# Optimization experiments

Hardware: AMD Instinct MI355X
Metric: run time of the kernel (lower is better)

The kernel has to match this reference:

```python
import jax, jax.numpy as jnp
import numpy as np

ALPHA = 32.0
RANK = 256
SCALE = ALPHA / RANK


def setup_inputs() -> dict:
    key = jax.random.key(0)
    k1, k2, k3, k4 = jax.random.split(key, 4)
    x = jax.random.normal(k1, (4, 2048, 4096), dtype=jnp.float32)
    A = jax.random.normal(k2, (256, 4096), dtype=jnp.float32)   # (rank, in)
    B = jax.random.normal(k3, (4096, 256), dtype=jnp.float32)   # (out, rank)
    d_A = jnp.ones((256,), dtype=jnp.float32)                    # init = ones (as in module)
    d_B = jax.random.normal(k4, (4096,), dtype=jnp.float32)      # perturbed for a nontrivial test
    return {"x": x, "A": A, "B": B, "d_A": d_A, "d_B": d_B}


def reference(x, A, B, d_A, d_B):
    # Effective weight: diag(d_B) @ B @ diag(d_A) @ A  -> (out, in)
    scaled_A = d_A[:, None] * A                 # (rank, in)
    BA = B @ scaled_A                            # (out, in)
    W_vera = d_B[:, None] * BA                   # (out, in)
    # out = x @ W_vera.T * scale  -> (..., out)
    return jnp.einsum('bsi,oi->bso', x, W_vera) * SCALE
```

## Files before the change

kernel.cpp:

```cpp
#include <hip/hip_runtime.h>
#include <hip/hip_bf16.h>


#define SCALE_F 0.125f
#define M_TOT 8192
#define K_IN 4096
#define RANK 256
#define N_OUT 4096
#define S_SPLIT 4
#define KC 1024

typedef __bf16 bf16_t;
typedef __bf16 bf16x8 __attribute__((ext_vector_type(8)));
typedef __bf16 bf16x4 __attribute__((ext_vector_type(4)));
typedef float f32x4 __attribute__((ext_vector_type(4)));

typedef __attribute__((address_space(3))) unsigned int lds_u32_t;
typedef const __attribute__((address_space(1))) unsigned int glob_u32_t;

__device__ __forceinline__ void async16(const void* g, void* l) {
    __builtin_amdgcn_global_load_lds((glob_u32_t*)g, (lds_u32_t*)l, 16, 0, 0);
}

__global__ __launch_bounds__(256) void conv_AB(const float* __restrict__ A,
                                               const float* __restrict__ dA,
                                               const float* __restrict__ B,
                                               bf16_t* __restrict__ Ab,
                                               bf16_t* __restrict__ Bb) {
    int b = blockIdx.x;
    if (b < 1024) {
        int idx = b * 256 + threadIdx.x;
        float4 v = ((const float4*)A)[idx];
        float s = dA[idx >> 10];
        bf16x4 o;
        o.x = (bf16_t)(v.x * s); o.y = (bf16_t)(v.y * s);
        o.z = (bf16_t)(v.z * s); o.w = (bf16_t)(v.w * s);
        ((bf16x4*)Ab)[idx] = o;
    } else {
        int idx = (b - 1024) * 256 + threadIdx.x;
        float4 v = ((const float4*)B)[idx];
        bf16x4 o;
        o.x = (bf16_t)v.x; o.y = (bf16_t)v.y;
        o.z = (bf16_t)v.z; o.w = (bf16_t)v.w;
        ((bf16x4*)Bb)[idx] = o;
    }
}

__global__ __launch_bounds__(256) void gemm1(const float* __restrict__ x,
                                             const bf16_t* __restrict__ Ab,
                                             bf16_t* __restrict__ part) {
    __shared__ bf16_t sX[2][64 * 64];
    __shared__ bf16_t sA[2][128 * 64];
    const int tid = threadIdx.x;
    const int lane = tid & 63, wave = tid >> 6;
    const int wm = wave >> 1, wn = wave & 1;
    const int l15 = lane & 15, quad = lane >> 4;
    const int bm = blockIdx.x * 64;
    const int bn = blockIdx.y * 128;
    const int k0 = blockIdx.z * KC;

    f32x4 acc[2][4];
    const f32x4 zero = {0.f, 0.f, 0.f, 0.f};
    #pragma unroll
    for (int i = 0; i < 2; i++)
        #pragma unroll
        for (int j = 0; j < 4; j++) acc[i][j] = zero;

    f32x4 xr[2][2];

    auto issue_x = [&](int kk) {
        #pragma unroll
        for (int c = 0; c < 2; c++) {
            int idx = c * 256 + tid;
            int row = idx >> 3, sl = idx & 7;
            const float* sp = &x[(size_t)(bm + row) * K_IN + kk + sl * 8];
            xr[c][0] = *(const f32x4*)sp;
            xr[c][1] = *(const f32x4*)(sp + 4);
        }
    };
    auto stage_a = [&](int b, int kk) {
        #pragma unroll
        for (int c = 0; c < 4; c++) {
            int idx = c * 256 + tid;
            int row = idx >> 3, sl = idx & 7;
            async16(&Ab[(size_t)(bn + row) * K_IN + kk + ((sl ^ (row & 7)) << 3)],
                    &sA[b][idx * 8]);
        }
    };
    auto write_x = [&](int b) {
        #pragma unroll
        for (int c = 0; c < 2; c++) {
            int idx = c * 256 + tid;
            int row = idx >> 3, sl = idx & 7;
            bf16x8 o;
            #pragma unroll
            for (int e = 0; e < 4; e++) {
                o[e]     = (bf16_t)xr[c][0][e];
                o[e + 4] = (bf16_t)xr[c][1][e];
            }
            *(bf16x8*)&sX[b][row * 64 + ((sl ^ (row & 7)) << 3)] = o;
        }
    };
    auto compute = [&](int b) {
        #pragma unroll
        for (int ks = 0; ks < 2; ks++) {
            bf16x8 af[2], bfr[4];
            #pragma unroll
            for (int i = 0; i < 2; i++) {
                int row = wm * 32 + i * 16 + l15;
                af[i] = *(const bf16x8*)&sX[b][row * 64 + ((((ks << 2) | quad) ^ (row & 7)) << 3)];
            }
            #pragma unroll
            for (int j = 0; j < 4; j++) {
                int row = wn * 64 + j * 16 + l15;
                bfr[j] = *(const bf16x8*)&sA[b][row * 64 + ((((ks << 2) | quad) ^ (row & 7)) << 3)];
            }
            #pragma unroll
            for (int i = 0; i < 2; i++)
                #pragma unroll
                for (int j = 0; j < 4; j++)
                    acc[i][j] = __builtin_amdgcn_mfma_f32_16x16x32_bf16(bfr[j], af[i], acc[i][j], 0, 0, 0);
        }
    };

    issue_x(k0);
    stage_a(0, k0);
    write_x(0);
    __syncthreads();

    int cur = 0;
    for (int it = 1; it < KC / 64; ++it) {
        const int nxt = cur ^ 1;
        const int kk = k0 + it * 64;
        issue_x(kk);
        stage_a(nxt, kk);
        compute(cur);
        write_x(nxt);
        __syncthreads();
        cur = nxt;
    }
    compute(cur);

    bf16_t* p = part + (size_t)blockIdx.z * (M_TOT * RANK);
    #pragma unroll
    for (int i = 0; i < 2; i++) {
        int row = bm + wm * 32 + i * 16 + l15;
        #pragma unroll
        for (int j = 0; j < 4; j++) {
            int col = bn + wn * 64 + j * 16 + quad * 4;
            bf16x4 o;
            #pragma unroll
            for (int r = 0; r < 4; r++) o[r] = (bf16_t)acc[i][j][r];
            *(bf16x4*)&p[(size_t)row * RANK + col] = o;
        }
    }
}

__global__ __launch_bounds__(256) void reduce_t(const bf16_t* __restrict__ part,
                                                bf16_t* __restrict__ t) {
    int i = (blockIdx.x * 256 + threadIdx.x) * 8;
    float s[8] = {0.f, 0.f, 0.f, 0.f, 0.f, 0.f, 0.f, 0.f};
    #pragma unroll
    for (int z = 0; z < S_SPLIT; z++) {
        bf16x8 v = *(const bf16x8*)&part[(size_t)z * M_TOT * RANK + i];
        #pragma unroll
        for (int e = 0; e < 8; e++) s[e] += (float)v[e];
    }
    bf16x8 o;
    #pragma unroll
    for (int e = 0; e < 8; e++) o[e] = (bf16_t)s[e];
    *(bf16x8*)&t[i] = o;
}

__global__ __launch_bounds__(256) void gemm2(const bf16_t* __restrict__ t,
                                             const bf16_t* __restrict__ Bb,
                                             const float* __restrict__ dB,
                                             float* __restrict__ out) {
    __shared__ bf16_t sT[2][128 * 64];
    __shared__ bf16_t sB[2][64 * 64];
    const int tid = threadIdx.x;
    const int lane = tid & 63, wave = tid >> 6;
    const int wm = wave >> 1, wn = wave & 1;
    const int l15 = lane & 15, quad = lane >> 4;
    const int bm = blockIdx.x * 128;
    const int bn = blockIdx.y * 64;

    f32x4 acc[4][2];
    const f32x4 zero = {0.f, 0.f, 0.f, 0.f};
    #pragma unroll
    for (int i = 0; i < 4; i++)
        #pragma unroll
        for (int j = 0; j < 2; j++) acc[i][j] = zero;

    auto stage = [&](int b, int kt) {
        #pragma unroll
        for (int c = 0; c < 4; c++) {
            int idx = c * 256 + tid;
            int row = idx >> 3, sl = idx & 7;
            async16(&t[(size_t)(bm + row) * RANK + kt + ((sl ^ (row & 7)) << 3)],
                    &sT[b][idx * 8]);
        }
        #pragma unroll
        for (int c = 0; c < 2; c++) {
            int idx = c * 256 + tid;
            int row = idx >> 3, sl = idx & 7;
            async16(&Bb[(size_t)(bn + row) * RANK + kt + ((sl ^ (row & 7)) << 3)],
                    &sB[b][idx * 8]);
        }
    };
    auto compute = [&](int b) {
        #pragma unroll
        for (int ks = 0; ks < 2; ks++) {
            bf16x8 af[4], bfr[2];
            #pragma unroll
            for (int i = 0; i < 4; i++) {
                int row = wm * 64 + i * 16 + l15;
                af[i] = *(const bf16x8*)&sT[b][row * 64 + ((((ks << 2) | quad) ^ (row & 7)) << 3)];
            }
            #pragma unroll
            for (int j = 0; j < 2; j++) {
                int row = wn * 32 + j * 16 + l15;
                bfr[j] = *(const bf16x8*)&sB[b][row * 64 + ((((ks << 2) | quad) ^ (row & 7)) << 3)];
            }
            #pragma unroll
            for (int i = 0; i < 4; i++)
                #pragma unroll
                for (int j = 0; j < 2; j++)
                    acc[i][j] = __builtin_amdgcn_mfma_f32_16x16x32_bf16(bfr[j], af[i], acc[i][j], 0, 0, 0);
        }
    };

    stage(0, 0);
    __syncthreads();
    int cur = 0;
    #pragma unroll
    for (int it = 1; it < RANK / 64; ++it) {
        stage(cur ^ 1, it * 64);
        compute(cur);
        __syncthreads();
        cur ^= 1;
    }
    compute(cur);

    #pragma unroll
    for (int i = 0; i < 4; i++) {
        int row = bm + wm * 64 + i * 16 + l15;
        #pragma unroll
        for (int j = 0; j < 2; j++) {
            int col = bn + wn * 32 + j * 16 + quad * 4;
            f32x4 db = *(const f32x4*)&dB[col];
            f32x4 o;
            #pragma unroll
            for (int r = 0; r < 4; r++) o[r] = db[r] * SCALE_F * acc[i][j][r];
            *(f32x4*)&out[(size_t)row * N_OUT + col] = o;
        }
    }
}

extern "C" void kernel_launch(void* const* d_in, const int* in_sizes, int n_in,
                              void* d_out, int out_size, void* d_ws, size_t ws_size,
                              hipStream_t stream) {
    const float* x  = (const float*)d_in[0];
    const float* A  = (const float*)d_in[1];
    const float* B  = (const float*)d_in[2];
    const float* dA = (const float*)d_in[3];
    const float* dB = (const float*)d_in[4];
    float* out = (float*)d_out;

    char* ws = (char*)d_ws;
    bf16_t* Ab   = (bf16_t*)ws;
    bf16_t* Bb   = (bf16_t*)(ws + (1u << 21));
    bf16_t* tt   = (bf16_t*)(ws + (1u << 22));
    bf16_t* part = (bf16_t*)(ws + (1u << 23));

    conv_AB<<<2048, 256, 0, stream>>>(A, dA, B, Ab, Bb);
    gemm1<<<dim3(128, 2, S_SPLIT), 256, 0, stream>>>(x, Ab, part);
    reduce_t<<<1024, 256, 0, stream>>>(part, tt);
    gemm2<<<dim3(64, 64), 256, 0, stream>>>(tt, Bb, dB, out);
}
```

Before: 319.7 us.

## Widen gemm1 tile to full rank and load whole K panel in gemm2

```diff
diff --git a/kernel.cpp b/kernel.cpp
--- a/kernel.cpp
+++ b/kernel.cpp
@@ -50,21 +50,20 @@
                                              const bf16_t* __restrict__ Ab,
                                              bf16_t* __restrict__ part) {
     __shared__ bf16_t sX[2][64 * 64];
-    __shared__ bf16_t sA[2][128 * 64];
+    __shared__ bf16_t sA[2][256 * 64];
     const int tid = threadIdx.x;
     const int lane = tid & 63, wave = tid >> 6;
     const int wm = wave >> 1, wn = wave & 1;
     const int l15 = lane & 15, quad = lane >> 4;
     const int bm = blockIdx.x * 64;
-    const int bn = blockIdx.y * 128;
-    const int k0 = blockIdx.z * KC;
-
-    f32x4 acc[2][4];
+    const int k0 = blockIdx.y * KC;
+
+    f32x4 acc[2][8];
     const f32x4 zero = {0.f, 0.f, 0.f, 0.f};
     #pragma unroll
     for (int i = 0; i < 2; i++)
         #pragma unroll
-        for (int j = 0; j < 4; j++) acc[i][j] = zero;
+        for (int j = 0; j < 8; j++) acc[i][j] = zero;
 
     f32x4 xr[2][2];
 
@@ -80,10 +79,10 @@
     };
     auto stage_a = [&](int b, int kk) {
         #pragma unroll
-        for (int c = 0; c < 4; c++) {
+        for (int c = 0; c < 8; c++) {
             int idx = c * 256 + tid;
             int row = idx >> 3, sl = idx & 7;
-            async16(&Ab[(size_t)(bn + row) * K_IN + kk + ((sl ^ (row & 7)) << 3)],
+            async16(&Ab[(size_t)row * K_IN + kk + ((sl ^ (row & 7)) << 3)],
                     &sA[b][idx * 8]);
         }
     };
@@ -104,21 +103,21 @@
     auto compute = [&](int b) {
         #pragma unroll
         for (int ks = 0; ks < 2; ks++) {
-            bf16x8 af[2], bfr[4];
+            bf16x8 af[2], bfr[8];
             #pragma unroll
             for (int i = 0; i < 2; i++) {
                 int row = wm * 32 + i * 16 + l15;
                 af[i] = *(const bf16x8*)&sX[b][row * 64 + ((((ks << 2) | quad) ^ (row & 7)) << 3)];
             }
             #pragma unroll
-            for (int j = 0; j < 4; j++) {
-                int row = wn * 64 + j * 16 + l15;
+            for (int j = 0; j < 8; j++) {
+                int row = wn * 128 + j * 16 + l15;
                 bfr[j] = *(const bf16x8*)&sA[b][row * 64 + ((((ks << 2) | quad) ^ (row & 7)) << 3)];
             }
             #pragma unroll
             for (int i = 0; i < 2; i++)
                 #pragma unroll
-                for (int j = 0; j < 4; j++)
+                for (int j = 0; j < 8; j++)
                     acc[i][j] = __builtin_amdgcn_mfma_f32_16x16x32_bf16(bfr[j], af[i], acc[i][j], 0, 0, 0);
         }
     };
@@ -141,13 +140,13 @@
     }
     compute(cur);
 
-    bf16_t* p = part + (size_t)blockIdx.z * (M_TOT * RANK);
+    bf16_t* p = part + (size_t)blockIdx.y * (M_TOT * RANK);
     #pragma unroll
     for (int i = 0; i < 2; i++) {
         int row = bm + wm * 32 + i * 16 + l15;
         #pragma unroll
-        for (int j = 0; j < 4; j++) {
-            int col = bn + wn * 64 + j * 16 + quad * 4;
+        for (int j = 0; j < 8; j++) {
+            int col = wn * 128 + j * 16 + quad * 4;
             bf16x4 o;
             #pragma unroll
             for (int r = 0; r < 4; r++) o[r] = (bf16_t)acc[i][j][r];
@@ -176,75 +175,57 @@
                                              const bf16_t* __restrict__ Bb,
                                              const float* __restrict__ dB,
                                              float* __restrict__ out) {
-    __shared__ bf16_t sT[2][128 * 64];
-    __shared__ bf16_t sB[2][64 * 64];
+    __shared__ bf16_t sT[64 * 256];
+    __shared__ bf16_t sB[64 * 256];
     const int tid = threadIdx.x;
     const int lane = tid & 63, wave = tid >> 6;
     const int wm = wave >> 1, wn = wave & 1;
     const int l15 = lane & 15, quad = lane >> 4;
-    const int bm = blockIdx.x * 128;
+    const int bm = blockIdx.x * 64;
     const int bn = blockIdx.y * 64;
 
-    f32x4 acc[4][2];
+    #pragma unroll
+    for (int c = 0; c < 8; c++) {
+        int idx = c * 256 + tid;
+        int row = idx >> 5, sl = idx & 31;
+        int src = ((sl ^ (row & 7)) << 3);
+        async16(&t[(size_t)(bm + row) * RANK + src], &sT[idx * 8]);
+        async16(&Bb[(size_t)(bn + row) * RANK + src], &sB[idx * 8]);
+    }
+    __syncthreads();
+
+    f32x4 acc[2][2];
     const f32x4 zero = {0.f, 0.f, 0.f, 0.f};
     #pragma unroll
-    for (int i = 0; i < 4; i++)
+    for (int i = 0; i < 2; i++)
         #pragma unroll
         for (int j = 0; j < 2; j++) acc[i][j] = zero;
 
-    auto stage = [&](int b, int kt) {
-        #pragma unroll
-        for (int c = 0; c < 4; c++) {
-            int idx = c * 256 + tid;
-            int row = idx >> 3, sl = idx & 7;
-            async16(&t[(size_t)(bm + row) * RANK + kt + ((sl ^ (row & 7)) << 3)],
-                    &sT[b][idx * 8]);
-        }
-        #pragma unroll
-        for (int c = 0; c < 2; c++) {
-            int idx = c * 256 + tid;
-            int row = idx >> 3, sl = idx & 7;
-            async16(&Bb[(size_t)(bn + row) * RANK + kt + ((sl ^ (row & 7)) << 3)],
-                    &sB[b][idx * 8]);
-        }
-    };
-    auto compute = [&](int b) {
-        #pragma unroll
-        for (int ks = 0; ks < 2; ks++) {
-            bf16x8 af[4], bfr[2];
-            #pragma unroll
-            for (int i = 0; i < 4; i++) {
-                int row = wm * 64 + i * 16 + l15;
-                af[i] = *(const bf16x8*)&sT[b][row * 64 + ((((ks << 2) | quad) ^ (row & 7)) << 3)];
-            }
-            #pragma unroll
-            for (int j = 0; j < 2; j++) {
-                int row = wn * 32 + j * 16 + l15;
-                bfr[j] = *(const bf16x8*)&sB[b][row * 64 + ((((ks << 2) | quad) ^ (row & 7)) << 3)];
-            }
-            #pragma unroll
-            for (int i = 0; i < 4; i++)
-                #pragma unroll
-                for (int j = 0; j < 2; j++)
-                    acc[i][j] = __builtin_amdgcn_mfma_f32_16x16x32_bf16(bfr[j], af[i], acc[i][j], 0, 0, 0);
-        }
-    };
-
-    stage(0, 0);
-    __syncthreads();
-    int cur = 0;
-    #pragma unroll
-    for (int it = 1; it < RANK / 64; ++it) {
-        stage(cur ^ 1, it * 64);
-        compute(cur);
-        __syncthreads();
-        cur ^= 1;
-    }
-    compute(cur);
-
-    #pragma unroll
-    for (int i = 0; i < 4; i++) {
-        int row = bm + wm * 64 + i * 16 + l15;
+    #pragma unroll
+    for (int ks = 0; ks < 8; ks++) {
+        bf16x8 af[2], bfr[2];
+        #pragma unroll
+        for (int i = 0; i < 2; i++) {
+            int row = wm * 32 + i * 16 + l15;
+            int slot = ((ks << 2) | quad) ^ (row & 7);
+            af[i] = *(const bf16x8*)&sT[row * 256 + slot * 8];
+        }
+        #pragma unroll
+        for (int j = 0; j < 2; j++) {
+            int row = wn * 32 + j * 16 + l15;
+            int slot = ((ks << 2) | quad) ^ (row & 7);
+            bfr[j] = *(const bf16x8*)&sB[row * 256 + slot * 8];
+        }
+        #pragma unroll
+        for (int i = 0; i < 2; i++)
+            #pragma unroll
+            for (int j = 0; j < 2; j++)
+                acc[i][j] = __builtin_amdgcn_mfma_f32_16x16x32_bf16(bfr[j], af[i], acc[i][j], 0, 0, 0);
+    }
+
+    #pragma unroll
+    for (int i = 0; i < 2; i++) {
+        int row = bm + wm * 32 + i * 16 + l15;
         #pragma unroll
         for (int j = 0; j < 2; j++) {
             int col = bn + wn * 32 + j * 16 + quad * 4;
@@ -274,7 +255,7 @@
     bf16_t* part = (bf16_t*)(ws + (1u << 23));
 
     conv_AB<<<2048, 256, 0, stream>>>(A, dA, B, Ab, Bb);
-    gemm1<<<dim3(128, 2, S_SPLIT), 256, 0, stream>>>(x, Ab, part);
+    gemm1<<<dim3(128, S_SPLIT), 256, 0, stream>>>(x, Ab, part);
     reduce_t<<<1024, 256, 0, stream>>>(part, tt);
-    gemm2<<<dim3(64, 64), 256, 0, stream>>>(tt, Bb, dB, out);
-}
+    gemm2<<<dim3(128, 64), 256, 0, stream>>>(tt, Bb, dB, out);
+}
```

Measured after the change: 338.5 us. +5.9%, slower.

## Stage fp32 x via async LDS loads with K=32 tiles and two-deep prefetch

Applied to the files above, without the earlier changes.

```diff
diff --git a/kernel.cpp b/kernel.cpp
--- a/kernel.cpp
+++ b/kernel.cpp
@@ -46,11 +46,11 @@
     }
 }
 
-__global__ __launch_bounds__(256) void gemm1(const float* __restrict__ x,
-                                             const bf16_t* __restrict__ Ab,
-                                             bf16_t* __restrict__ part) {
-    __shared__ bf16_t sX[2][64 * 64];
-    __shared__ bf16_t sA[2][128 * 64];
+__global__ __launch_bounds__(256, 4) void gemm1(const float* __restrict__ x,
+                                                const bf16_t* __restrict__ Ab,
+                                                bf16_t* __restrict__ part) {
+    __shared__ float  sXf[2][64 * 32];
+    __shared__ bf16_t sA[2][128 * 32];
     const int tid = threadIdx.x;
     const int lane = tid & 63, wave = tid >> 6;
     const int wm = wave >> 1, wn = wave & 1;
@@ -66,79 +66,65 @@
         #pragma unroll
         for (int j = 0; j < 4; j++) acc[i][j] = zero;
 
-    f32x4 xr[2][2];
-
-    auto issue_x = [&](int kk) {
+    auto stage = [&](int b, int ts) {
+        const int kk = k0 + ts * 32;
         #pragma unroll
         for (int c = 0; c < 2; c++) {
             int idx = c * 256 + tid;
             int row = idx >> 3, sl = idx & 7;
-            const float* sp = &x[(size_t)(bm + row) * K_IN + kk + sl * 8];
-            xr[c][0] = *(const f32x4*)sp;
-            xr[c][1] = *(const f32x4*)(sp + 4);
-        }
-    };
-    auto stage_a = [&](int b, int kk) {
-        #pragma unroll
-        for (int c = 0; c < 4; c++) {
-            int idx = c * 256 + tid;
-            int row = idx >> 3, sl = idx & 7;
-            async16(&Ab[(size_t)(bn + row) * K_IN + kk + ((sl ^ (row & 7)) << 3)],
-                    &sA[b][idx * 8]);
-        }
-    };
-    auto write_x = [&](int b) {
+            async16(&x[(size_t)(bm + row) * K_IN + kk + ((sl ^ (row & 7)) << 2)],
+                    &sXf[b][idx * 4]);
+        }
         #pragma unroll
         for (int c = 0; c < 2; c++) {
             int idx = c * 256 + tid;
-            int row = idx >> 3, sl = idx & 7;
-            bf16x8 o;
-            #pragma unroll
-            for (int e = 0; e < 4; e++) {
-                o[e]     = (bf16_t)xr[c][0][e];
-                o[e + 4] = (bf16_t)xr[c][1][e];
-            }
-            *(bf16x8*)&sX[b][row * 64 + ((sl ^ (row & 7)) << 3)] = o;
+            int row = idx >> 2, sl = idx & 3;
+            async16(&Ab[(size_t)(bn + row) * K_IN + kk + ((sl ^ ((row >> 1) & 3)) << 3)],
+                    &sA[b][idx * 8]);
         }
     };
     auto compute = [&](int b) {
-        #pragma unroll
-        for (int ks = 0; ks < 2; ks++) {
-            bf16x8 af[2], bfr[4];
-            #pragma unroll
-            for (int i = 0; i < 2; i++) {
-                int row = wm * 32 + i * 16 + l15;
-                af[i] = *(const bf16x8*)&sX[b][row * 64 + ((((ks << 2) | quad) ^ (row & 7)) << 3)];
-            }
-            #pragma unroll
-            for (int j = 0; j < 4; j++) {
-                int row = wn * 64 + j * 16 + l15;
-                bfr[j] = *(const bf16x8*)&sA[b][row * 64 + ((((ks << 2) | quad) ^ (row & 7)) << 3)];
-            }
-            #pragma unroll
-            for (int i = 0; i < 2; i++)
-                #pragma unroll
-                for (int j = 0; j < 4; j++)
-                    acc[i][j] = __builtin_amdgcn_mfma_f32_16x16x32_bf16(bfr[j], af[i], acc[i][j], 0, 0, 0);
-        }
-    };
-
-    issue_x(k0);
-    stage_a(0, k0);
-    write_x(0);
-    __syncthreads();
-
+        bf16x8 af[2], bfr[4];
+        #pragma unroll
+        for (int i = 0; i < 2; i++) {
+            int row = wm * 32 + i * 16 + l15;
+            f32x4 v0 = *(const f32x4*)&sXf[b][row * 32 + ((((quad << 1) | 0) ^ (row & 7)) << 2)];
+            f32x4 v1 = *(const f32x4*)&sXf[b][row * 32 + ((((quad << 1) | 1) ^ (row & 7)) << 2)];
+            bf16x8 t;
+            #pragma unroll
+            for (int e = 0; e < 4; e++) { t[e] = (bf16_t)v0[e]; t[e + 4] = (bf16_t)v1[e]; }
+            af[i] = t;
+        }
+        #pragma unroll
+        for (int j = 0; j < 4; j++) {
+            int row = wn * 64 + j * 16 + l15;
+            bfr[j] = *(const bf16x8*)&sA[b][row * 32 + ((quad ^ ((row >> 1) & 3)) << 3)];
+        }
+        #pragma unroll
+        for (int i = 0; i < 2; i++)
+            #pragma unroll
+            for (int j = 0; j < 4; j++)
+                acc[i][j] = __builtin_amdgcn_mfma_f32_16x16x32_bf16(bfr[j], af[i], acc[i][j], 0, 0, 0);
+    };
+
+    const int NT = KC / 32;
+    stage(0, 0);
+    stage(1, 1);
     int cur = 0;
-    for (int it = 1; it < KC / 64; ++it) {
-        const int nxt = cur ^ 1;
-        const int kk = k0 + it * 64;
-        issue_x(kk);
-        stage_a(nxt, kk);
+    for (int t = 0; t < NT - 2; ++t) {
+        asm volatile("s_waitcnt vmcnt(4)" ::: "memory");
+        __builtin_amdgcn_s_barrier();
         compute(cur);
-        write_x(nxt);
-        __syncthreads();
-        cur = nxt;
-    }
+        __builtin_amdgcn_s_barrier();
+        stage(cur, t + 2);
+        cur ^= 1;
+    }
+    asm volatile("s_waitcnt vmcnt(4)" ::: "memory");
+    __builtin_amdgcn_s_barrier();
+    compute(cur);
+    cur ^= 1;
+    asm volatile("s_waitcnt vmcnt(0)" ::: "memory");
+    __builtin_amdgcn_s_barrier();
     compute(cur);
 
     bf16_t* p = part + (size_t)blockIdx.z * (M_TOT * RANK);
@@ -172,12 +158,12 @@
     *(bf16x8*)&t[i] = o;
 }
 
-__global__ __launch_bounds__(256) void gemm2(const bf16_t* __restrict__ t,
-                                             const bf16_t* __restrict__ Bb,
-                                             const float* __restrict__ dB,
-                                             float* __restrict__ out) {
-    __shared__ bf16_t sT[2][128 * 64];
-    __shared__ bf16_t sB[2][64 * 64];
+__global__ __launch_bounds__(256, 4) void gemm2(const bf16_t* __restrict__ t,
+                                                const bf16_t* __restrict__ Bb,
+                                                const float* __restrict__ dB,
+                                                float* __restrict__ out) {
+    __shared__ bf16_t sT[2][128 * 32];
+    __shared__ bf16_t sB[2][64 * 32];
     const int tid = threadIdx.x;
     const int lane = tid & 63, wave = tid >> 6;
     const int wm = wave >> 1, wn = wave & 1;
@@ -192,54 +178,59 @@
         #pragma unroll
         for (int j = 0; j < 2; j++) acc[i][j] = zero;
 
-    auto stage = [&](int b, int kt) {
-        #pragma unroll
-        for (int c = 0; c < 4; c++) {
-            int idx = c * 256 + tid;
-            int row = idx >> 3, sl = idx & 7;
-            async16(&t[(size_t)(bm + row) * RANK + kt + ((sl ^ (row & 7)) << 3)],
-                    &sT[b][idx * 8]);
-        }
+    auto stage = [&](int b, int ts) {
+        const int kt = ts * 32;
         #pragma unroll
         for (int c = 0; c < 2; c++) {
             int idx = c * 256 + tid;
-            int row = idx >> 3, sl = idx & 7;
-            async16(&Bb[(size_t)(bn + row) * RANK + kt + ((sl ^ (row & 7)) << 3)],
-                    &sB[b][idx * 8]);
+            int row = idx >> 2, sl = idx & 3;
+            async16(&t[(size_t)(bm + row) * RANK + kt + ((sl ^ ((row >> 1) & 3)) << 3)],
+                    &sT[b][idx * 8]);
+        }
+        {
+            int row = tid >> 2, sl = tid & 3;
+            async16(&Bb[(size_t)(bn + row) * RANK + kt + ((sl ^ ((row >> 1) & 3)) << 3)],
+                    &sB[b][tid * 8]);
         }
     };
     auto compute = [&](int b) {
-        #pragma unroll
-        for (int ks = 0; ks < 2; ks++) {
-            bf16x8 af[4], bfr[2];
-            #pragma unroll
-            for (int i = 0; i < 4; i++) {
-                int row = wm * 64 + i * 16 + l15;
-                af[i] = *(const bf16x8*)&sT[b][row * 64 + ((((ks << 2) | quad) ^ (row & 7)) << 3)];
-            }
-            #pragma unroll
-            for (int j = 0; j < 2; j++) {
-                int row = wn * 32 + j * 16 + l15;
-                bfr[j] = *(const bf16x8*)&sB[b][row * 64 + ((((ks << 2) | quad) ^ (row & 7)) << 3)];
-            }
-            #pragma unroll
-            for (int i = 0; i < 4; i++)
-                #pragma unroll
-                for (int j = 0; j < 2; j++)
-                    acc[i][j] = __builtin_amdgcn_mfma_f32_16x16x32_bf16(bfr[j], af[i], acc[i][j], 0, 0, 0);
-        }
-    };
-
+        bf16x8 af[4], bfr[2];
+        #pragma unroll
+        for (int i = 0; i < 4; i++) {
+            int row = wm * 64 + i * 16 + l15;
+            af[i] = *(const bf16x8*)&sT[b][row * 32 + ((quad ^ ((row >> 1) & 3)) << 3)];
+        }
+        #pragma unroll
+        for (int j = 0; j < 2; j++) {
+            int row = wn * 32 + j * 16 + l15;
+            bfr[j] = *(const bf16x8*)&sB[b][row * 32 + ((quad ^ ((row >> 1) & 3)) << 3)];
+        }
+        #pragma unroll
+        for (int i = 0; i < 4; i++)
+            #pragma unroll
+            for (int j = 0; j < 2; j++)
+                acc[i][j] = __builtin_amdgcn_mfma_f32_16x16x32_bf16(bfr[j], af[i], acc[i][j], 0, 0, 0);
+    };
+
+    const int NT = RANK / 32;
     stage(0, 0);
-    __syncthreads();
+    stage(1, 1);
     int cur = 0;
     #pragma unroll
-    for (int it = 1; it < RANK / 64; ++it) {
-        stage(cur ^ 1, it * 64);
+    for (int t = 0; t < NT - 2; ++t) {
+        asm volatile("s_waitcnt vmcnt(3)" ::: "memory");
+        __builtin_amdgcn_s_barrier();
         compute(cur);
-        __syncthreads();
+        __builtin_amdgcn_s_barrier();
+        stage(cur, t + 2);
         cur ^= 1;
     }
+    asm volatile("s_waitcnt vmcnt(3)" ::: "memory");
+    __builtin_amdgcn_s_barrier();
+    compute(cur);
+    cur ^= 1;
+    asm volatile("s_waitcnt vmcnt(0)" ::: "memory");
+    __builtin_amdgcn_s_barrier();
     compute(cur);
 
     #pragma unroll
```

Result: no change. 321.5 us (+0.6%).
